# Kernel tuning notes

Measured on AMD Instinct MI355X. Metric: run time of the kernel, lower is better.

The kernel has to match this reference:

```python
import jax, jax.numpy as jnp
import numpy as np

B, C, S, DIM = 8, 3, 1024, 768
H = 3
HD = DIM // H  # 256


def setup_inputs() -> dict:
    key = jax.random.key(0)
    ks = jax.random.split(key, 7)
    s = 1.0 / np.sqrt(HD)  # torch Linear default init scale
    return {
        "linear_embed": jax.random.normal(ks[0], (B, C, S, DIM), dtype=jnp.float32),
        "Wq": jax.random.uniform(ks[1], (H, HD, HD), jnp.float32, -s, s),
        "bq": jax.random.uniform(ks[2], (H, HD), jnp.float32, -s, s),
        "Wk": jax.random.uniform(ks[3], (H, HD, HD), jnp.float32, -s, s),
        "bk": jax.random.uniform(ks[4], (H, HD), jnp.float32, -s, s),
        "Wv": jax.random.uniform(ks[5], (H, HD, HD), jnp.float32, -s, s),
        "bv": jax.random.uniform(ks[6], (H, HD), jnp.float32, -s, s),
    }


def reference(linear_embed, Wq, bq, Wk, bk, Wv, bv):
    # Split last dim into heads: [B, C, S, H, HD]
    x = linear_embed.reshape(B, C, S, H, HD)
    # Per-head Linear: y = x @ W.T + b (torch convention, W is [out, in])
    q = jnp.einsum("bcshd,hed->bcshe", x, Wq) + bq
    k = jnp.einsum("bcshd,hed->bcshe", x, Wk) + bk
    v = jnp.einsum("bcshd,hed->bcshe", x, Wv) + bv
    scale = 1.0 / np.sqrt(HD)
    scores = jnp.einsum("bcshe,bcthe->bchst", q, k) * scale  # [B,C,H,S,S]
    attn = jax.nn.softmax(scores, axis=-1)
    out = jnp.einsum("bchst,bcthe->bcshe", attn, v)  # [B,C,S,H,HD]
    # hstack over heads -> [B,C,S,DIM]; hstack over channels -> [B,S,C*DIM]
    out = out.reshape(B, C, S, DIM)
    return jnp.transpose(out, (0, 2, 1, 3)).reshape(B, S, C * DIM)
```

## Files before the change

### kernel.cpp

```cpp
#include <hip/hip_runtime.h>

#define Bn 8
#define Cn 3
#define Sn 1024
#define DIMn 768
#define Hn 3
#define HDn 256
#define BCHn 72
#define SnHD (Sn*HDn)

typedef __bf16 bf16x8 __attribute__((ext_vector_type(8)));
typedef float f32x4 __attribute__((ext_vector_type(4)));
typedef float f32x16 __attribute__((ext_vector_type(16)));
typedef unsigned short u16x8 __attribute__((ext_vector_type(8)));
typedef unsigned short u16x4 __attribute__((ext_vector_type(4)));
typedef unsigned u32x2 __attribute__((ext_vector_type(2)));
typedef unsigned u32x4 __attribute__((ext_vector_type(4)));

static __device__ __forceinline__ unsigned short f2bf(float f){
  unsigned u = __builtin_bit_cast(unsigned, f);
  u += 0x7fffu + ((u >> 16) & 1u);
  return (unsigned short)(u >> 16);
}
static __device__ __forceinline__ unsigned pk2(float a, float b){
  return (unsigned)f2bf(a) | ((unsigned)f2bf(b) << 16);
}
static __device__ __forceinline__ u16x4 cvt4(float4 v){
  u16x4 r = { f2bf(v.x), f2bf(v.y), f2bf(v.z), f2bf(v.w) };
  return r;
}
static __device__ __forceinline__ u16x8 cvt8(float4 a, float4 b){
  u16x8 r = { f2bf(a.x), f2bf(a.y), f2bf(a.z), f2bf(a.w),
              f2bf(b.x), f2bf(b.y), f2bf(b.z), f2bf(b.w) };
  return r;
}
static __device__ __forceinline__ bf16x8 ld8(const void* p){
  return __builtin_bit_cast(bf16x8, *(const u16x8*)p);
}
static __device__ __forceinline__ float fexp2(float x){
#if __has_builtin(__builtin_amdgcn_exp2f)
  return __builtin_amdgcn_exp2f(x);
#else
  return exp2f(x);
#endif
}

#if __has_builtin(__builtin_amdgcn_global_load_lds)
#define HAVE_ASYNC 1
static __device__ __forceinline__ void async16(const void* g, void* l){
  __builtin_amdgcn_global_load_lds((const __attribute__((address_space(1))) void*)g,
                                   (__attribute__((address_space(3))) void*)l, 16, 0, 0);
}
#else
#define HAVE_ASYNC 0
#endif

static __device__ __forceinline__ bf16x8 pack8(const float* t, int hi){
  unsigned A0 = pk2(t[0], t[1]), A1 = pk2(t[2], t[3]);
  unsigned B0 = pk2(t[4], t[5]), B1 = pk2(t[6], t[7]);
#if __has_builtin(__builtin_amdgcn_permlane32_swap)
  u32x2 r0 = __builtin_amdgcn_permlane32_swap(A0, B0, false, false);
  u32x2 r1 = __builtin_amdgcn_permlane32_swap(A1, B1, false, false);
  u32x4 w = { r0[0], r1[0], r0[1], r1[1] };
#else
  unsigned sA0 = (unsigned)__shfl_xor((int)A0, 32), sA1 = (unsigned)__shfl_xor((int)A1, 32);
  unsigned sB0 = (unsigned)__shfl_xor((int)B0, 32), sB1 = (unsigned)__shfl_xor((int)B1, 32);
  u32x4 w = { hi ? sB0 : A0, hi ? sB1 : A1, hi ? B0 : sA0, hi ? B1 : sA1 };
#endif
  (void)hi;
  return __builtin_bit_cast(bf16x8, w);
}

__global__ __launch_bounds__(256) void wprep(
    const float* __restrict__ Wq, const float* __restrict__ Wk, const float* __restrict__ Wv,
    unsigned short* __restrict__ Wb)
{
  const int which = blockIdx.z, h = blockIdx.y;
  const float* src = which == 0 ? Wq : (which == 1 ? Wk : Wv);
  const float scale = (which == 0) ? 0.09016844136545405f : 1.0f;
  const int off = blockIdx.x*1024 + threadIdx.x*4;
  float4 v = *(const float4*)(src + (long)h*65536 + off);
  v.x *= scale; v.y *= scale; v.z *= scale; v.w *= scale;
  const int e = off >> 8, k0 = off & 255;
  const int ks = k0 >> 6, kst = (k0 >> 4) & 3, hb = (k0 >> 3) & 1, j0 = k0 & 7;
  const long o = (long)(which*Hn + h)*65536 + ks*16384
               + ((e>>5)*4 + kst)*512 + (((hb<<5)|(e&31))*8) + j0;
  *(u16x4*)(Wb + o) = cvt4(v);
}

__global__ __launch_bounds__(256, 2) void projkv(
    const float* __restrict__ x, const unsigned short* __restrict__ Wb,
    const float* __restrict__ bk, const float* __restrict__ bv,
    unsigned short* __restrict__ Kw, unsigned short* __restrict__ Vt)
{
  __shared__ alignas(16) char SM[16384];

  const int tid = threadIdx.x, lane = tid & 63, wave = tid >> 6;
  const int l31 = lane & 31, hi = lane >> 5;
  const int tg = wave >> 1, eh = wave & 1;
  const int bch = blockIdx.y;
  const int h = bch % Hn, c = (bch / Hn) % Cn, b = bch / (Hn*Cn);
  const int tb = blockIdx.x * 64;
  const long xb_ = ((long)(b*Cn + c)*Sn + tb)*DIMn + h*HDn;
  const unsigned short* Wkb = Wb + (long)(1*Hn + h)*65536;
  const unsigned short* Wvb = Wb + (long)(2*Hn + h)*65536;

  float4 xr[2][2];
  auto loadX = [&](int ks){
    #pragma unroll
    for (int i = 0; i < 2; ++i){
      const int vid = tid + i*256;
      const int t = vid >> 3, kg = vid & 7;
      const float* p = x + xb_ + (long)t*DIMn + ks*64 + kg*8;
      xr[i][0] = *(const float4*)p;
      xr[i][1] = *(const float4*)(p + 4);
    }
  };
  loadX(0);

  f32x16 accK[4] = {}, accV[4] = {};
  for (int ks = 0; ks < 4; ++ks){
    const int buf = ks & 1;
    #pragma unroll
    for (int i = 0; i < 2; ++i){
      const int vid = tid + i*256;
      const int t = vid >> 3, kg = vid & 7;
      *(u16x8*)(SM + buf*8192 + t*128 + ((kg*16) ^ ((t & 7) << 4))) = cvt8(xr[i][0], xr[i][1]);
    }
    __syncthreads();
    if (ks < 3) loadX(ks + 1);
    #pragma unroll
    for (int kst = 0; kst < 4; ++kst){
      bf16x8 wk2[4], wv2[4];
      #pragma unroll
      for (int et = 0; et < 4; ++et){
        const long wo = (long)ks*16384 + ((eh*4 + et)*4 + kst)*512 + lane*8;
        wk2[et] = ld8(Wkb + wo);
        wv2[et] = ld8(Wvb + wo);
      }
      bf16x8 xf = ld8(SM + buf*8192 + (tg*32 + l31)*128 + ((kst*32 + hi*16) ^ ((l31 & 7) << 4)));
      #pragma unroll
      for (int et = 0; et < 4; ++et){
        accK[et] = __builtin_amdgcn_mfma_f32_32x32x16_bf16(wk2[et], xf, accK[et], 0, 0, 0);
        accV[et] = __builtin_amdgcn_mfma_f32_32x32x16_bf16(xf, wv2[et], accV[et], 0, 0, 0);
      }
    }
  }

  const int ttile = blockIdx.x*2 + tg;
  {
    unsigned short* Kg = Kw + (long)bch*SnHD + (long)ttile*8192;
    const float* bkh = bk + h*HDn + eh*128;
    #pragma unroll
    for (int et = 0; et < 4; ++et){
      float tt[16];
      #pragma unroll
      for (int G = 0; G < 4; ++G){
        const float4 bb = *(const float4*)(bkh + et*32 + 8*G + 4*hi);
        tt[4*G+0] = accK[et][4*G+0] + bb.x;
        tt[4*G+1] = accK[et][4*G+1] + bb.y;
        tt[4*G+2] = accK[et][4*G+2] + bb.z;
        tt[4*G+3] = accK[et][4*G+3] + bb.w;
      }
      *(u16x8*)(Kg + (eh*8 + et*2 + 0)*512 + lane*8) = __builtin_bit_cast(u16x8, pack8(tt,     hi));
      *(u16x8*)(Kg + (eh*8 + et*2 + 1)*512 + lane*8) = __builtin_bit_cast(u16x8, pack8(tt + 8, hi));
    }
  }
  {
    unsigned short* Vg = Vt + (long)bch*SnHD + (long)ttile*8192;
    #pragma unroll
    for (int et = 0; et < 4; ++et){
      const float bs = bv[h*HDn + eh*128 + et*32 + l31];
      float tt[16];
      #pragma unroll
      for (int r = 0; r < 16; ++r) tt[r] = accV[et][r] + bs;
      *(u16x8*)(Vg + ((eh*4 + et)*2 + 0)*512 + lane*8) = __builtin_bit_cast(u16x8, pack8(tt,     hi));
      *(u16x8*)(Vg + ((eh*4 + et)*2 + 1)*512 + lane*8) = __builtin_bit_cast(u16x8, pack8(tt + 8, hi));
    }
  }
}

__global__ __launch_bounds__(256, 2) void attn(
    const float* __restrict__ x, const unsigned short* __restrict__ Wb,
    const float* __restrict__ bq,
    const unsigned short* __restrict__ Kw, const unsigned short* __restrict__ Vt,
    float* __restrict__ out)
{
  __shared__ alignas(16) char SM[65536];

  const int tid = threadIdx.x, lane = tid & 63, wave = tid >> 6;
  const int l31 = lane & 31, hi = lane >> 5;
  const int bid = blockIdx.x;
  const int g = bid >> 3;
  const int bch = (g & ~7) | (bid & 7);
  const int qt = g & 7;
  const int h = bch % Hn, c = (bch / Hn) % Cn, b = bch / (Hn*Cn);
  const int q0 = qt * 128;
  const long xb_ = ((long)(b*Cn + c)*Sn + q0)*DIMn + h*HDn;

  float4 xv[4][2];
  auto loadX = [&](int ks){
    #pragma unroll
    for (int i = 0; i < 4; ++i){
      const int vid = tid + i*256;
      const int q = vid >> 3, kg = vid & 7;
      const float* p = x + xb_ + (long)q*DIMn + ks*64 + kg*8;
      xv[i][0] = *(const float4*)p;
      xv[i][1] = *(const float4*)(p + 4);
    }
  };
  const unsigned short* Wq2 = Wb + (long)h*65536;
  auto issueW = [&](int ks){
    #pragma unroll
    for (int i = 0; i < 8; ++i){
      const int f = wave*8 + i;
#if HAVE_ASYNC
      async16(Wq2 + (long)ks*16384 + f*512 + lane*8, SM + 16384 + f*1024);
#else
      *(u16x8*)(SM + 16384 + f*1024 + lane*16) =
          *(const u16x8*)(Wq2 + (long)ks*16384 + f*512 + lane*8);
#endif
    }
  };
  loadX(0);
  f32x16 acc[8] = {};
  for (int ks = 0; ks < 4; ++ks){
    #pragma unroll
    for (int i = 0; i < 4; ++i){
      const int vid = tid + i*256;
      const int q = vid >> 3, kg = vid & 7;
      *(u16x8*)(SM + q*128 + ((kg*16) ^ ((q & 7) << 4))) = cvt8(xv[i][0], xv[i][1]);
    }
    issueW(ks);
    __syncthreads();
    if (ks < 3) loadX(ks + 1);
    #pragma unroll
    for (int kst = 0; kst < 4; ++kst){
      bf16x8 xb = ld8(SM + (wave*32 + l31)*128 + ((kst*32 + hi*16) ^ ((l31 & 7) << 4)));
      #pragma unroll
      for (int et = 0; et < 8; ++et){
        bf16x8 af = ld8(SM + 16384 + (et*4 + kst)*1024 + lane*16);
        acc[et] = __builtin_amdgcn_mfma_f32_32x32x16_bf16(af, xb, acc[et], 0, 0, 0);
      }
    }
    __syncthreads();
  }

  const unsigned short* Kb = Kw + (long)bch*SnHD;
  const unsigned short* Vb = Vt + (long)bch*SnHD;
  auto stageKV = [&](int jt, int buf){
    const long kb2 = (long)jt * 8192;
    #pragma unroll
    for (int i = 0; i < 4; ++i){
      const int f = wave*4 + i;
#if HAVE_ASYNC
      async16(Kb + kb2 + f*512 + lane*8, SM + buf*16384 + f*1024);
#else
      *(u16x8*)(SM + buf*16384 + f*1024 + lane*16) = *(const u16x8*)(Kb + kb2 + f*512 + lane*8);
#endif
    }
    #pragma unroll
    for (int i = 0; i < 4; ++i){
      const int f = wave*4 + i;
#if HAVE_ASYNC
      async16(Vb + kb2 + f*512 + lane*8, SM + 32768 + buf*16384 + f*1024);
#else
      *(u16x8*)(SM + 32768 + buf*16384 + f*1024 + lane*16) = *(const u16x8*)(Vb + kb2 + f*512 + lane*8);
#endif
    }
  };
  stageKV(0, 0);

  const float s2 = 0.09016844136545405f;
  const float* bqh = bq + h*HDn;
  bf16x8 qf[16];
  #pragma unroll
  for (int et = 0; et < 8; ++et){
    float t[16];
    #pragma unroll
    for (int G = 0; G < 4; ++G){
      const float4 bb = *(const float4*)(bqh + et*32 + 8*G + 4*hi);
      t[4*G+0] = fmaf(bb.x, s2, acc[et][4*G+0]);
      t[4*G+1] = fmaf(bb.y, s2, acc[et][4*G+1]);
      t[4*G+2] = fmaf(bb.z, s2, acc[et][4*G+2]);
      t[4*G+3] = fmaf(bb.w, s2, acc[et][4*G+3]);
    }
    qf[2*et]   = pack8(t,     hi);
    qf[2*et+1] = pack8(t + 8, hi);
  }
  __syncthreads();

  f32x16 o[8] = {};
  float lsum = 0.f;
  #pragma unroll 2
  for (int jt = 0; jt < 32; ++jt){
    const int buf = jt & 1;
    if (jt < 31) stageKV(jt + 1, buf ^ 1);
    f32x16 s0 = {}, s1 = {};
    const char* KLb = SM + buf*16384 + lane*16;
    #pragma unroll
    for (int kc = 0; kc < 8; ++kc){
      bf16x8 k0 = ld8(KLb + (2*kc+0)*1024);
      s0 = __builtin_amdgcn_mfma_f32_32x32x16_bf16(k0, qf[2*kc+0], s0, 0, 0, 0);
      bf16x8 k1 = ld8(KLb + (2*kc+1)*1024);
      s1 = __builtin_amdgcn_mfma_f32_32x32x16_bf16(k1, qf[2*kc+1], s1, 0, 0, 0);
    }
    const char* VLb = SM + 32768 + buf*16384 + lane*16;
    float p[16];
    #pragma unroll
    for (int i = 0; i < 8; ++i) p[i] = fexp2(s0[i] + s1[i]);
    bf16x8 pB0 = pack8(p, hi);
    #pragma unroll
    for (int et = 0; et < 8; ++et){
      bf16x8 v0 = ld8(VLb + (et*2+0)*1024);
      o[et] = __builtin_amdgcn_mfma_f32_32x32x16_bf16(v0, pB0, o[et], 0, 0, 0);
    }
    #pragma unroll
    for (int i = 8; i < 16; ++i) p[i] = fexp2(s0[i] + s1[i]);
    bf16x8 pB1 = pack8(p + 8, hi);
    #pragma unroll
    for (int et = 0; et < 8; ++et){
      bf16x8 v1 = ld8(VLb + (et*2+1)*1024);
      o[et] = __builtin_amdgcn_mfma_f32_32x32x16_bf16(v1, pB1, o[et], 0, 0, 0);
    }
    lsum += (((p[0]+p[1])+(p[2]+p[3])) + ((p[4]+p[5])+(p[6]+p[7])))
          + (((p[8]+p[9])+(p[10]+p[11])) + ((p[12]+p[13])+(p[14]+p[15])));
    __syncthreads();
  }

  const float lt = lsum + __shfl_xor(lsum, 32);
  const float inv = 1.0f / lt;
  #pragma unroll
  for (int et = 0; et < 8; ++et)
    #pragma unroll
    for (int r = 0; r < 16; ++r) o[et][r] *= inv;

  char* TB = SM + wave*16384;
  #pragma unroll
  for (int pass = 0; pass < 2; ++pass){
    #pragma unroll
    for (int e2 = 0; e2 < 4; ++e2){
      const int et = pass*4 + e2;
      #pragma unroll
      for (int G = 0; G < 4; ++G){
        f32x4 w = { o[et][4*G+0], o[et][4*G+1], o[et][4*G+2], o[et][4*G+3] };
        const int el0 = e2*32 + 8*G + 4*hi;
        *(f32x4*)(TB + l31*512 + ((el0*4) ^ ((l31 & 7) << 4))) = w;
      }
    }
    #pragma unroll
    for (int i = 0; i < 16; ++i){
      const int qr = i*2 + hi;
      f32x4 v = *(const f32x4*)(TB + qr*512 + ((l31*16) ^ ((qr & 7) << 4)));
      float* op = out + ((long)(b*Sn + q0 + wave*32 + qr)*Cn + c)*DIMn + h*HDn + pass*128 + l31*4;
      *(f32x4*)op = v;
    }
  }
}

extern "C" void kernel_launch(void* const* d_in, const int* in_sizes, int n_in,
                              void* d_out, int out_size, void* d_ws, size_t ws_size,
                              hipStream_t stream) {
  const float* x  = (const float*)d_in[0];
  const float* Wq = (const float*)d_in[1];
  const float* bq = (const float*)d_in[2];
  const float* Wk = (const float*)d_in[3];
  const float* bk = (const float*)d_in[4];
  const float* Wv = (const float*)d_in[5];
  const float* bv = (const float*)d_in[6];
  float* out = (float*)d_out;
  unsigned short* Kw = (unsigned short*)d_ws;
  unsigned short* Vt = Kw + (size_t)BCHn * SnHD;
  unsigned short* Wb = Vt + (size_t)BCHn * SnHD;

  wprep<<<dim3(64, Hn, 3), 256, 0, stream>>>(Wq, Wk, Wv, Wb);
  projkv<<<dim3(16, BCHn), 256, 0, stream>>>(x, Wb, bk, bv, Kw, Vt);
  attn<<<dim3(BCHn * 8), 256, 0, stream>>>(x, Wb, bq, Kw, Vt, out);
}
```

Baseline: 344.1 us.

## Prefetch K/V two chunks ahead with explicit vmcnt waits and MFMA priority

```diff
diff --git a/kernel.cpp b/kernel.cpp
--- a/kernel.cpp
+++ b/kernel.cpp
@@ -54,6 +54,8 @@
 #else
 #define HAVE_ASYNC 0
 #endif
+
+#define WAITV(N) asm volatile("s_waitcnt vmcnt(" #N ")" ::: "memory")
 
 static __device__ __forceinline__ bf16x8 pack8(const float* t, int hi){
   unsigned A0 = pk2(t[0], t[1]), A1 = pk2(t[2], t[3]);
@@ -186,7 +188,7 @@
     const unsigned short* __restrict__ Kw, const unsigned short* __restrict__ Vt,
     float* __restrict__ out)
 {
-  __shared__ alignas(16) char SM[65536];
+  __shared__ alignas(16) char SM[66560];
 
   const int tid = threadIdx.x, lane = tid & 63, wave = tid >> 6;
   const int l31 = lane & 31, hi = lane >> 5;
@@ -198,6 +200,9 @@
   const int q0 = qt * 128;
   const long xb_ = ((long)(b*Cn + c)*Sn + q0)*DIMn + h*HDn;
 
+  float* bql = (float*)(SM + 65536);
+  bql[tid] = bq[h*HDn + tid] * 0.09016844136545405f;
+
   float4 xv[4][2];
   auto loadX = [&](int ks){
     #pragma unroll
@@ -270,34 +275,30 @@
     }
   };
   stageKV(0, 0);
-
-  const float s2 = 0.09016844136545405f;
-  const float* bqh = bq + h*HDn;
+  stageKV(1, 1);
+
   bf16x8 qf[16];
   #pragma unroll
   for (int et = 0; et < 8; ++et){
     float t[16];
     #pragma unroll
     for (int G = 0; G < 4; ++G){
-      const float4 bb = *(const float4*)(bqh + et*32 + 8*G + 4*hi);
-      t[4*G+0] = fmaf(bb.x, s2, acc[et][4*G+0]);
-      t[4*G+1] = fmaf(bb.y, s2, acc[et][4*G+1]);
-      t[4*G+2] = fmaf(bb.z, s2, acc[et][4*G+2]);
-      t[4*G+3] = fmaf(bb.w, s2, acc[et][4*G+3]);
+      const f32x4 bb = *(const f32x4*)&bql[et*32 + 8*G + 4*hi];
+      t[4*G+0] = acc[et][4*G+0] + bb[0];
+      t[4*G+1] = acc[et][4*G+1] + bb[1];
+      t[4*G+2] = acc[et][4*G+2] + bb[2];
+      t[4*G+3] = acc[et][4*G+3] + bb[3];
     }
     qf[2*et]   = pack8(t,     hi);
     qf[2*et+1] = pack8(t + 8, hi);
   }
-  __syncthreads();
 
   f32x16 o[8] = {};
   float lsum = 0.f;
-  #pragma unroll 2
-  for (int jt = 0; jt < 32; ++jt){
-    const int buf = jt & 1;
-    if (jt < 31) stageKV(jt + 1, buf ^ 1);
+  auto doChunk = [&](int buf){
     f32x16 s0 = {}, s1 = {};
     const char* KLb = SM + buf*16384 + lane*16;
+    __builtin_amdgcn_s_setprio(1);
     #pragma unroll
     for (int kc = 0; kc < 8; ++kc){
       bf16x8 k0 = ld8(KLb + (2*kc+0)*1024);
@@ -305,28 +306,57 @@
       bf16x8 k1 = ld8(KLb + (2*kc+1)*1024);
       s1 = __builtin_amdgcn_mfma_f32_32x32x16_bf16(k1, qf[2*kc+1], s1, 0, 0, 0);
     }
+    __builtin_amdgcn_s_setprio(0);
     const char* VLb = SM + 32768 + buf*16384 + lane*16;
     float p[16];
     #pragma unroll
     for (int i = 0; i < 8; ++i) p[i] = fexp2(s0[i] + s1[i]);
     bf16x8 pB0 = pack8(p, hi);
+    __builtin_amdgcn_s_setprio(1);
     #pragma unroll
     for (int et = 0; et < 8; ++et){
       bf16x8 v0 = ld8(VLb + (et*2+0)*1024);
       o[et] = __builtin_amdgcn_mfma_f32_32x32x16_bf16(v0, pB0, o[et], 0, 0, 0);
     }
+    __builtin_amdgcn_s_setprio(0);
     #pragma unroll
     for (int i = 8; i < 16; ++i) p[i] = fexp2(s0[i] + s1[i]);
     bf16x8 pB1 = pack8(p + 8, hi);
+    __builtin_amdgcn_s_setprio(1);
     #pragma unroll
     for (int et = 0; et < 8; ++et){
       bf16x8 v1 = ld8(VLb + (et*2+1)*1024);
       o[et] = __builtin_amdgcn_mfma_f32_32x32x16_bf16(v1, pB1, o[et], 0, 0, 0);
     }
+    __builtin_amdgcn_s_setprio(0);
     lsum += (((p[0]+p[1])+(p[2]+p[3])) + ((p[4]+p[5])+(p[6]+p[7])))
           + (((p[8]+p[9])+(p[10]+p[11])) + ((p[12]+p[13])+(p[14]+p[15])));
-    __syncthreads();
-  }
+  };
+
+  for (int jt = 0; jt < 31; ++jt){
+    const int buf = jt & 1;
+    WAITV(8);
+#if !HAVE_ASYNC
+    asm volatile("s_waitcnt lgkmcnt(0)" ::: "memory");
+#endif
+    __builtin_amdgcn_s_barrier();
+    asm volatile("" ::: "memory");
+    doChunk(buf);
+    asm volatile("" ::: "memory");
+    __builtin_amdgcn_s_barrier();
+    asm volatile("" ::: "memory");
+    if (jt < 30) stageKV(jt + 2, buf);
+  }
+  WAITV(0);
+#if !HAVE_ASYNC
+  asm volatile("s_waitcnt lgkmcnt(0)" ::: "memory");
+#endif
+  __builtin_amdgcn_s_barrier();
+  asm volatile("" ::: "memory");
+  doChunk(31 & 1);
+  asm volatile("" ::: "memory");
+  __builtin_amdgcn_s_barrier();
+  asm volatile("" ::: "memory");
 
   const float lt = lsum + __shfl_xor(lsum, 32);
   const float inv = 1.0f / lt;
```

Result: no change. 349.0 us (+1.4%).

## Read V directly from global, double-buffer K further ahead, prefetch weights in registers

Applied to the files above, without the earlier changes.

```diff
diff --git a/kernel.cpp b/kernel.cpp
--- a/kernel.cpp
+++ b/kernel.cpp
@@ -25,10 +25,6 @@
 static __device__ __forceinline__ unsigned pk2(float a, float b){
   return (unsigned)f2bf(a) | ((unsigned)f2bf(b) << 16);
 }
-static __device__ __forceinline__ u16x4 cvt4(float4 v){
-  u16x4 r = { f2bf(v.x), f2bf(v.y), f2bf(v.z), f2bf(v.w) };
-  return r;
-}
 static __device__ __forceinline__ u16x8 cvt8(float4 a, float4 b){
   u16x8 r = { f2bf(a.x), f2bf(a.y), f2bf(a.z), f2bf(a.w),
               f2bf(b.x), f2bf(b.y), f2bf(b.z), f2bf(b.w) };
@@ -75,17 +71,18 @@
     const float* __restrict__ Wq, const float* __restrict__ Wk, const float* __restrict__ Wv,
     unsigned short* __restrict__ Wb)
 {
-  const int which = blockIdx.z, h = blockIdx.y;
+  const int ks = blockIdx.x, eb = blockIdx.y, wh = blockIdx.z;
+  const int which = wh / Hn, h = wh % Hn;
   const float* src = which == 0 ? Wq : (which == 1 ? Wk : Wv);
   const float scale = (which == 0) ? 0.09016844136545405f : 1.0f;
-  const int off = blockIdx.x*1024 + threadIdx.x*4;
-  float4 v = *(const float4*)(src + (long)h*65536 + off);
-  v.x *= scale; v.y *= scale; v.z *= scale; v.w *= scale;
-  const int e = off >> 8, k0 = off & 255;
-  const int ks = k0 >> 6, kst = (k0 >> 4) & 3, hb = (k0 >> 3) & 1, j0 = k0 & 7;
-  const long o = (long)(which*Hn + h)*65536 + ks*16384
-               + ((e>>5)*4 + kst)*512 + (((hb<<5)|(e&31))*8) + j0;
-  *(u16x4*)(Wb + o) = cvt4(v);
+  const int lane = threadIdx.x & 63, kst = threadIdx.x >> 6;
+  const int e = eb*32 + (lane & 31);
+  const int d0 = ks*64 + kst*16 + (lane >> 5)*8;
+  const float* sp = src + (long)h*65536 + e*256 + d0;
+  float4 a = *(const float4*)sp, b = *(const float4*)(sp + 4);
+  a.x *= scale; a.y *= scale; a.z *= scale; a.w *= scale;
+  b.x *= scale; b.y *= scale; b.z *= scale; b.w *= scale;
+  *(u16x8*)(Wb + (long)wh*65536 + ks*16384 + (eb*4 + kst)*512 + lane*8) = cvt8(a, b);
 }
 
 __global__ __launch_bounds__(256, 2) void projkv(
@@ -118,6 +115,18 @@
   };
   loadX(0);
 
+  bf16x8 wkr[2][4], wvr[2][4];
+  auto loadW = [&](int kk, int pb){
+    const int ks2 = kk >> 2, kst2 = kk & 3;
+    #pragma unroll
+    for (int et = 0; et < 4; ++et){
+      const long wo = (long)ks2*16384 + ((eh*4 + et)*4 + kst2)*512 + lane*8;
+      wkr[pb][et] = ld8(Wkb + wo);
+      wvr[pb][et] = ld8(Wvb + wo);
+    }
+  };
+  loadW(0, 0);
+
   f32x16 accK[4] = {}, accV[4] = {};
   for (int ks = 0; ks < 4; ++ks){
     const int buf = ks & 1;
@@ -131,18 +140,13 @@
     if (ks < 3) loadX(ks + 1);
     #pragma unroll
     for (int kst = 0; kst < 4; ++kst){
-      bf16x8 wk2[4], wv2[4];
+      const int pb = kst & 1;
+      if (ks < 3 || kst < 3) loadW(ks*4 + kst + 1, pb ^ 1);
+      bf16x8 xf = ld8(SM + buf*8192 + (tg*32 + l31)*128 + ((kst*32 + hi*16) ^ ((l31 & 7) << 4)));
       #pragma unroll
       for (int et = 0; et < 4; ++et){
-        const long wo = (long)ks*16384 + ((eh*4 + et)*4 + kst)*512 + lane*8;
-        wk2[et] = ld8(Wkb + wo);
-        wv2[et] = ld8(Wvb + wo);
-      }
-      bf16x8 xf = ld8(SM + buf*8192 + (tg*32 + l31)*128 + ((kst*32 + hi*16) ^ ((l31 & 7) << 4)));
-      #pragma unroll
-      for (int et = 0; et < 4; ++et){
-        accK[et] = __builtin_amdgcn_mfma_f32_32x32x16_bf16(wk2[et], xf, accK[et], 0, 0, 0);
-        accV[et] = __builtin_amdgcn_mfma_f32_32x32x16_bf16(xf, wv2[et], accV[et], 0, 0, 0);
+        accK[et] = __builtin_amdgcn_mfma_f32_32x32x16_bf16(wkr[pb][et], xf, accK[et], 0, 0, 0);
+        accV[et] = __builtin_amdgcn_mfma_f32_32x32x16_bf16(xf, wvr[pb][et], accV[et], 0, 0, 0);
       }
     }
   }
@@ -186,7 +190,7 @@
     const unsigned short* __restrict__ Kw, const unsigned short* __restrict__ Vt,
     float* __restrict__ out)
 {
-  __shared__ alignas(16) char SM[65536];
+  __shared__ alignas(16) char SM[66560];
 
   const int tid = threadIdx.x, lane = tid & 63, wave = tid >> 6;
   const int l31 = lane & 31, hi = lane >> 5;
@@ -198,6 +202,9 @@
   const int q0 = qt * 128;
   const long xb_ = ((long)(b*Cn + c)*Sn + q0)*DIMn + h*HDn;
 
+  float* bql = (float*)(SM + 65536);
+  bql[tid] = bq[h*HDn + tid] * 0.09016844136545405f;
+
   float4 xv[4][2];
   auto loadX = [&](int ks){
     #pragma unroll
@@ -248,7 +255,7 @@
 
   const unsigned short* Kb = Kw + (long)bch*SnHD;
   const unsigned short* Vb = Vt + (long)bch*SnHD;
-  auto stageKV = [&](int jt, int buf){
+  auto stageK = [&](int jt, int buf){
     const long kb2 = (long)jt * 8192;
     #pragma unroll
     for (int i = 0; i < 4; ++i){
@@ -259,31 +266,21 @@
       *(u16x8*)(SM + buf*16384 + f*1024 + lane*16) = *(const u16x8*)(Kb + kb2 + f*512 + lane*8);
 #endif
     }
-    #pragma unroll
-    for (int i = 0; i < 4; ++i){
-      const int f = wave*4 + i;
-#if HAVE_ASYNC
-      async16(Vb + kb2 + f*512 + lane*8, SM + 32768 + buf*16384 + f*1024);
-#else
-      *(u16x8*)(SM + 32768 + buf*16384 + f*1024 + lane*16) = *(const u16x8*)(Vb + kb2 + f*512 + lane*8);
-#endif
-    }
-  };
-  stageKV(0, 0);
-
-  const float s2 = 0.09016844136545405f;
-  const float* bqh = bq + h*HDn;
+  };
+  stageK(0, 0);
+  stageK(1, 1);
+
   bf16x8 qf[16];
   #pragma unroll
   for (int et = 0; et < 8; ++et){
     float t[16];
     #pragma unroll
     for (int G = 0; G < 4; ++G){
-      const float4 bb = *(const float4*)(bqh + et*32 + 8*G + 4*hi);
-      t[4*G+0] = fmaf(bb.x, s2, acc[et][4*G+0]);
-      t[4*G+1] = fmaf(bb.y, s2, acc[et][4*G+1]);
-      t[4*G+2] = fmaf(bb.z, s2, acc[et][4*G+2]);
-      t[4*G+3] = fmaf(bb.w, s2, acc[et][4*G+3]);
+      const f32x4 bb = *(const f32x4*)&bql[et*32 + 8*G + 4*hi];
+      t[4*G+0] = acc[et][4*G+0] + bb[0];
+      t[4*G+1] = acc[et][4*G+1] + bb[1];
+      t[4*G+2] = acc[et][4*G+2] + bb[2];
+      t[4*G+3] = acc[et][4*G+3] + bb[3];
     }
     qf[2*et]   = pack8(t,     hi);
     qf[2*et+1] = pack8(t + 8, hi);
@@ -295,9 +292,9 @@
   #pragma unroll 2
   for (int jt = 0; jt < 32; ++jt){
     const int buf = jt & 1;
-    if (jt < 31) stageKV(jt + 1, buf ^ 1);
     f32x16 s0 = {}, s1 = {};
     const char* KLb = SM + buf*16384 + lane*16;
+    __builtin_amdgcn_s_setprio(1);
     #pragma unroll
     for (int kc = 0; kc < 8; ++kc){
       bf16x8 k0 = ld8(KLb + (2*kc+0)*1024);
@@ -305,27 +302,28 @@
       bf16x8 k1 = ld8(KLb + (2*kc+1)*1024);
       s1 = __builtin_amdgcn_mfma_f32_32x32x16_bf16(k1, qf[2*kc+1], s1, 0, 0, 0);
     }
-    const char* VLb = SM + 32768 + buf*16384 + lane*16;
+    __builtin_amdgcn_s_setprio(0);
     float p[16];
     #pragma unroll
     for (int i = 0; i < 8; ++i) p[i] = fexp2(s0[i] + s1[i]);
     bf16x8 pB0 = pack8(p, hi);
     #pragma unroll
-    for (int et = 0; et < 8; ++et){
-      bf16x8 v0 = ld8(VLb + (et*2+0)*1024);
-      o[et] = __builtin_amdgcn_mfma_f32_32x32x16_bf16(v0, pB0, o[et], 0, 0, 0);
-    }
-    #pragma unroll
     for (int i = 8; i < 16; ++i) p[i] = fexp2(s0[i] + s1[i]);
     bf16x8 pB1 = pack8(p + 8, hi);
-    #pragma unroll
-    for (int et = 0; et < 8; ++et){
-      bf16x8 v1 = ld8(VLb + (et*2+1)*1024);
-      o[et] = __builtin_amdgcn_mfma_f32_32x32x16_bf16(v1, pB1, o[et], 0, 0, 0);
-    }
     lsum += (((p[0]+p[1])+(p[2]+p[3])) + ((p[4]+p[5])+(p[6]+p[7])))
           + (((p[8]+p[9])+(p[10]+p[11])) + ((p[12]+p[13])+(p[14]+p[15])));
+    const unsigned short* Vc = Vb + (long)jt*8192;
+    __builtin_amdgcn_s_setprio(1);
+    #pragma unroll
+    for (int et = 0; et < 8; ++et){
+      bf16x8 v0 = ld8(Vc + (et*2+0)*512 + lane*8);
+      o[et] = __builtin_amdgcn_mfma_f32_32x32x16_bf16(v0, pB0, o[et], 0, 0, 0);
+      bf16x8 v1 = ld8(Vc + (et*2+1)*512 + lane*8);
+      o[et] = __builtin_amdgcn_mfma_f32_32x32x16_bf16(v1, pB1, o[et], 0, 0, 0);
+    }
+    __builtin_amdgcn_s_setprio(0);
     __syncthreads();
+    if (jt < 30) stageK(jt + 2, buf);
   }
 
   const float lt = lsum + __shfl_xor(lsum, 32);
@@ -355,6 +353,7 @@
       float* op = out + ((long)(b*Sn + q0 + wave*32 + qr)*Cn + c)*DIMn + h*HDn + pass*128 + l31*4;
       *(f32x4*)op = v;
     }
+    if (pass == 0) __syncthreads();
   }
 }
 
@@ -373,7 +372,7 @@
   unsigned short* Vt = Kw + (size_t)BCHn * SnHD;
   unsigned short* Wb = Vt + (size_t)BCHn * SnHD;
 
-  wprep<<<dim3(64, Hn, 3), 256, 0, stream>>>(Wq, Wk, Wv, Wb);
+  wprep<<<dim3(4, 8, 9), 256, 0, stream>>>(Wq, Wk, Wv, Wb);
   projkv<<<dim3(16, BCHn), 256, 0, stream>>>(x, Wb, bk, bv, Kw, Vt);
   attn<<<dim3(BCHn * 8), 256, 0, stream>>>(x, Wb, bq, Kw, Vt, out);
 }
```

Result: slower. 587.3 us (+70.7%).
